# Kernel tuning notes

Hardware: AMD Instinct MI355X
Metric: run time of the kernel (lower is better)

Reference implementation:

```python
import jax, jax.numpy as jnp
import numpy as np

T = 16384
D_IN = 512
D_HID = 512
D_OUT = 512


def setup_inputs() -> dict:
    key = jax.random.key(0)
    ks = jax.random.split(key, 7)
    s_in = 1.0 / np.sqrt(D_IN)
    s_hid = 1.0 / np.sqrt(D_HID)
    xs = jax.random.normal(ks[0], (T, D_IN), dtype=jnp.float32)
    Wz = jax.random.uniform(ks[1], (D_HID, D_IN), jnp.float32, -s_in, s_in)
    bz = jax.random.uniform(ks[2], (D_HID,), jnp.float32, -s_in, s_in)
    Wh = jax.random.uniform(ks[3], (D_HID, D_IN), jnp.float32, -s_in, s_in)
    bh = jax.random.uniform(ks[4], (D_HID,), jnp.float32, -s_in, s_in)
    Wo = jax.random.uniform(ks[5], (D_OUT, D_HID), jnp.float32, -s_hid, s_hid)
    bo = jax.random.uniform(ks[6], (D_OUT,), jnp.float32, -s_hid, s_hid)
    return {"xs": xs, "Wz": Wz, "bz": bz, "Wh": Wh, "bh": bh, "Wo": Wo, "bo": bo}


def _combine(first, second):
    a0, b0 = first
    a1, b1 = second
    return (a0 * a1, a1 * b0 + b1)


def reference(xs, Wz, bz, Wh, bh, Wo, bo):
    # gates and candidate hidden states: [T, H]
    zs = jax.nn.sigmoid(xs @ Wz.T + bz)
    hs = xs @ Wh.T + bh
    # prepend identity element (a=1, b=0) for the h_0 = 0 initial state
    a = jnp.concatenate([jnp.ones((1, zs.shape[1]), zs.dtype), 1.0 - zs], axis=0)
    b = jnp.concatenate([jnp.zeros((1, zs.shape[1]), zs.dtype), zs * hs], axis=0)
    _, states = jax.lax.associative_scan(_combine, (a, b))  # [T+1, H]
    return states[1:] @ Wo.T + bo  # [T, D_OUT]
```

## Files before the change

### kernel.cpp

```cpp
#include <hip/hip_runtime.h>
#include <hip/hip_bf16.h>
#include <cstdint>
#include <cmath>

#define T_SEQ 16384
#define DMODEL 512
#define NCHUNK 512
#define LCHUNK 32
#define W_N    (DMODEL * DMODEL)
#define N4_W   (W_N / 4)
#define N4_W3  (3 * N4_W)

typedef __bf16 bf16x8 __attribute__((ext_vector_type(8)));
typedef float  f32x4  __attribute__((ext_vector_type(4)));

using bf16 = __hip_bfloat16;

__device__ __forceinline__ void load_lds16(const void* g, void* l) {
    __builtin_amdgcn_global_load_lds((const __attribute__((address_space(1))) void*)g,
                                     (__attribute__((address_space(3))) void*)l,
                                     16, 0, 0);
}

__device__ __forceinline__ unsigned short f2bf(float f) {
    union { float f; unsigned u; } v; v.f = f;
    const unsigned r = (v.u + 0x7FFFu + ((v.u >> 16) & 1u)) >> 16;
    return (unsigned short)r;
}
__device__ __forceinline__ float bf2f(unsigned short u) {
    union { unsigned u; float f; } v; v.u = ((unsigned)u) << 16;
    return v.f;
}

__device__ __forceinline__ void comb(float& A, float& B, float fA, float fB,
                                     float sA, float sB) {
    A = fA * sA;
    B = sA * fB + sB;
}

__global__ __launch_bounds__(256) void k_convert_w(
    const float* __restrict__ Wz, const float* __restrict__ Wh,
    const float* __restrict__ Wo,
    bf16* __restrict__ Wz_c, bf16* __restrict__ Wh_c, bf16* __restrict__ Wo_c)
{
    const int i = blockIdx.x * 256 + threadIdx.x;
    if (i >= N4_W3) return;
    const int w = i >> 16;
    const int o = i & 65535;
    const float* src = (w == 0) ? Wz : (w == 1) ? Wh : Wo;
    bf16* dst = (w == 0) ? Wz_c : (w == 1) ? Wh_c : Wo_c;
    const float4 v = ((const float4*)src)[o];
    ushort4 r;
    r.x = f2bf(v.x); r.y = f2bf(v.y); r.z = f2bf(v.z); r.w = f2bf(v.w);
    ((ushort4*)dst)[o] = r;
}

__global__ __launch_bounds__(256, 2) void gemm_zh(
    const float* __restrict__ xs, const bf16* __restrict__ Wz, const float* __restrict__ bz,
    const bf16* __restrict__ Wh, const float* __restrict__ bh,
    unsigned int* __restrict__ ab_ws,
    float* __restrict__ AaggT, float* __restrict__ BaggT)
{
    __shared__ __bf16 As[128 * 64];
    __shared__ __bf16 Zs[128 * 64];
    __shared__ __bf16 Hs[128 * 64];

    const int tid  = threadIdx.x;
    const int bm   = blockIdx.x;
    const int bn   = blockIdx.y;
    const int lane = tid & 63;
    const int wave = tid >> 6;
    const int wm   = wave >> 1;
    const int wn   = wave & 1;

    f32x4 accz[4][4], acch[4][4];
    #pragma unroll
    for (int i = 0; i < 4; ++i)
        #pragma unroll
        for (int j = 0; j < 4; ++j) {
            accz[i][j] = (f32x4){0.f, 0.f, 0.f, 0.f};
            acch[i][j] = (f32x4){0.f, 0.f, 0.f, 0.f};
        }

    const int row0 = tid >> 3;
    const int k8   = tid & 7;
    const bf16* zg = Wz + (size_t)(bn * 128) * DMODEL + k8 * 8;
    const bf16* hg = Wh + (size_t)(bn * 128) * DMODEL + k8 * 8;

    const int frow = tid >> 4;
    const int f4   = tid & 15;
    const float* xg = xs + ((size_t)(bm * 128) + frow) * DMODEL + f4 * 4;

    const int quad = lane >> 4;
    const int col  = lane & 15;

    for (int k0 = 0; k0 < DMODEL; k0 += 64) {
        #pragma unroll
        for (int it = 0; it < 4; ++it) {
            const int row   = row0 + it * 32;
            const int chunk = it * 256 + tid;
            load_lds16(zg + (size_t)row * DMODEL + k0, &Zs[chunk * 8]);
            load_lds16(hg + (size_t)row * DMODEL + k0, &Hs[chunk * 8]);
        }
        #pragma unroll
        for (int it2 = 0; it2 < 8; ++it2) {
            const int row = frow + it2 * 16;
            const float4 v = *(const float4*)(xg + (size_t)(it2 * 16) * DMODEL + k0);
            __hip_bfloat162 p0 = __float22bfloat162_rn(make_float2(v.x, v.y));
            __hip_bfloat162 p1 = __float22bfloat162_rn(make_float2(v.z, v.w));
            uint2 pk;
            pk.x = *(const unsigned*)&p0;
            pk.y = *(const unsigned*)&p1;
            *(uint2*)&As[row * 64 + f4 * 4] = pk;
        }
        __syncthreads();

        #pragma unroll
        for (int kk = 0; kk < 2; ++kk) {
            const int kb = kk * 32 + quad * 8;
            bf16x8 af[4], zf[4], hf[4];
            #pragma unroll
            for (int i = 0; i < 4; ++i) {
                const int am  = wm * 64 + i * 16 + col;
                const int bnr = wn * 64 + i * 16 + col;
                af[i] = *(const bf16x8*)&As[am * 64 + kb];
                zf[i] = *(const bf16x8*)&Zs[bnr * 64 + kb];
                hf[i] = *(const bf16x8*)&Hs[bnr * 64 + kb];
            }
            #pragma unroll
            for (int i = 0; i < 4; ++i)
                #pragma unroll
                for (int j = 0; j < 4; ++j) {
                    accz[i][j] = __builtin_amdgcn_mfma_f32_16x16x32_bf16(af[i], zf[j], accz[i][j], 0, 0, 0);
                    acch[i][j] = __builtin_amdgcn_mfma_f32_16x16x32_bf16(af[i], hf[j], acch[i][j], 0, 0, 0);
                }
        }
        __syncthreads();
    }

    const int c_lo = bm * 4 + wm * 2;
    #pragma unroll
    for (int j = 0; j < 4; ++j) {
        const int n = bn * 128 + wn * 64 + j * 16 + col;
        const float bzv = bz[n];
        const float bhv = bh[n];
        float cA[4], cB[4];
        #pragma unroll
        for (int i = 0; i < 4; ++i) {
            const int mbase = bm * 128 + wm * 64 + i * 16 + quad * 4;
            float A = 1.f, B = 0.f;
            #pragma unroll
            for (int r = 0; r < 4; ++r) {
                const float zpre = accz[i][j][r] + bzv;
                const float hpre = acch[i][j][r] + bhv;
                const float z = 1.f / (1.f + __expf(-zpre));
                const float a = 1.f - z;
                const float b = z * hpre;
                const size_t idx = (size_t)(mbase + r) * DMODEL + n;
                ab_ws[idx] = (unsigned)f2bf(a) | ((unsigned)f2bf(b) << 16);
                A = a * A;
                B = a * B + b;
            }
            cA[i] = A; cB[i] = B;
        }
        #pragma unroll
        for (int i = 0; i < 4; ++i) {
            float pA = __shfl_xor(cA[i], 16);
            float pB = __shfl_xor(cB[i], 16);
            const bool hi1 = quad & 1;
            comb(cA[i], cB[i], hi1 ? pA : cA[i], hi1 ? pB : cB[i],
                               hi1 ? cA[i] : pA, hi1 ? cB[i] : pB);
            pA = __shfl_xor(cA[i], 32);
            pB = __shfl_xor(cB[i], 32);
            const bool hi2 = quad >> 1;
            comb(cA[i], cB[i], hi2 ? pA : cA[i], hi2 ? pB : cB[i],
                               hi2 ? cA[i] : pA, hi2 ? cB[i] : pB);
        }
        float Alo, Blo, Ahi, Bhi;
        comb(Alo, Blo, cA[0], cB[0], cA[1], cB[1]);
        comb(Ahi, Bhi, cA[2], cB[2], cA[3], cB[3]);
        if (quad == 0) {
            AaggT[(size_t)n * NCHUNK + c_lo]     = Alo;
            BaggT[(size_t)n * NCHUNK + c_lo]     = Blo;
            AaggT[(size_t)n * NCHUNK + c_lo + 1] = Ahi;
            BaggT[(size_t)n * NCHUNK + c_lo + 1] = Bhi;
        }
    }
}

__global__ __launch_bounds__(512) void scan_p2(
    const float* __restrict__ AaggT, const float* __restrict__ BaggT,
    float* __restrict__ HpreT)
{
    const int h = blockIdx.x;
    const int c = threadIdx.x;
    __shared__ float sA[NCHUNK], sB[NCHUNK];

    float A = AaggT[(size_t)h * NCHUNK + c];
    float B = BaggT[(size_t)h * NCHUNK + c];
    sA[c] = A; sB[c] = B;
    __syncthreads();

    for (int off = 1; off < NCHUNK; off <<= 1) {
        float pA = 1.f, pB = 0.f;
        if (c >= off) { pA = sA[c - off]; pB = sB[c - off]; }
        __syncthreads();
        const float nB = A * pB + B;
        const float nA = A * pA;
        A = nA; B = nB;
        sA[c] = A; sB[c] = B;
        __syncthreads();
    }
    const float hp = (c == 0) ? 0.f : sB[c - 1];
    HpreT[(size_t)h * NCHUNK + c] = hp;
}

__global__ __launch_bounds__(256) void scan_p3(
    const unsigned int* __restrict__ ab_ws, const float* __restrict__ HpreT,
    unsigned short* __restrict__ states)
{
    const int tid = threadIdx.x;
    const int c   = blockIdx.x;
    float H0 = HpreT[(size_t)(2 * tid) * NCHUNK + c];
    float H1 = HpreT[(size_t)(2 * tid + 1) * NCHUNK + c];
    const size_t rowbase = (size_t)(c * LCHUNK) * DMODEL;
    #pragma unroll 8
    for (int i = 0; i < LCHUNK; ++i) {
        const size_t row = rowbase + (size_t)i * DMODEL;
        const uint2 u = ((const uint2*)(ab_ws + row))[tid];
        const float a0 = bf2f((unsigned short)(u.x & 0xFFFFu));
        const float b0 = bf2f((unsigned short)(u.x >> 16));
        const float a1 = bf2f((unsigned short)(u.y & 0xFFFFu));
        const float b1 = bf2f((unsigned short)(u.y >> 16));
        H0 = a0 * H0 + b0;
        H1 = a1 * H1 + b1;
        ushort2 s; s.x = f2bf(H0); s.y = f2bf(H1);
        ((ushort2*)(states + row))[tid] = s;
    }
}

__global__ __launch_bounds__(256, 2) void gemm_out(
    const bf16* __restrict__ states, const bf16* __restrict__ Wo, const float* __restrict__ bo,
    float* __restrict__ out)
{
    __shared__ __bf16 As[128 * 64];
    __shared__ __bf16 Bs[128 * 64];

    const int tid  = threadIdx.x;
    const int bm   = blockIdx.x;
    const int bn   = blockIdx.y;
    const int lane = tid & 63;
    const int wave = tid >> 6;
    const int wm   = wave >> 1;
    const int wn   = wave & 1;

    f32x4 acc[4][4];
    #pragma unroll
    for (int i = 0; i < 4; ++i)
        #pragma unroll
        for (int j = 0; j < 4; ++j)
            acc[i][j] = (f32x4){0.f, 0.f, 0.f, 0.f};

    const int row0 = tid >> 3;
    const int k8   = tid & 7;

    const bf16* ag = states + (size_t)(bm * 128) * DMODEL + k8 * 8;
    const bf16* bg = Wo     + (size_t)(bn * 128) * DMODEL + k8 * 8;

    const int quad = lane >> 4;
    const int col  = lane & 15;

    for (int k0 = 0; k0 < DMODEL; k0 += 64) {
        #pragma unroll
        for (int it = 0; it < 4; ++it) {
            const int row   = row0 + it * 32;
            const int chunk = it * 256 + tid;
            load_lds16(ag + (size_t)row * DMODEL + k0, &As[chunk * 8]);
            load_lds16(bg + (size_t)row * DMODEL + k0, &Bs[chunk * 8]);
        }
        __syncthreads();

        #pragma unroll
        for (int kk = 0; kk < 2; ++kk) {
            const int kb = kk * 32 + quad * 8;
            bf16x8 af[4], bf[4];
            #pragma unroll
            for (int i = 0; i < 4; ++i) {
                af[i] = *(const bf16x8*)&As[(wm * 64 + i * 16 + col) * 64 + kb];
                bf[i] = *(const bf16x8*)&Bs[(wn * 64 + i * 16 + col) * 64 + kb];
            }
            #pragma unroll
            for (int i = 0; i < 4; ++i)
                #pragma unroll
                for (int j = 0; j < 4; ++j)
                    acc[i][j] = __builtin_amdgcn_mfma_f32_16x16x32_bf16(af[i], bf[j], acc[i][j], 0, 0, 0);
        }
        __syncthreads();
    }

    #pragma unroll
    for (int j = 0; j < 4; ++j) {
        const int n = bn * 128 + wn * 64 + j * 16 + col;
        const float bov = bo[n];
        #pragma unroll
        for (int i = 0; i < 4; ++i) {
            const int mbase = bm * 128 + wm * 64 + i * 16 + quad * 4;
            #pragma unroll
            for (int r = 0; r < 4; ++r)
                out[(size_t)(mbase + r) * DMODEL + n] = acc[i][j][r] + bov;
        }
    }
}

extern "C" void kernel_launch(void* const* d_in, const int* in_sizes, int n_in,
                              void* d_out, int out_size, void* d_ws, size_t ws_size,
                              hipStream_t stream)
{
    const float* xs = (const float*)d_in[0];
    const float* Wz = (const float*)d_in[1];
    const float* bz = (const float*)d_in[2];
    const float* Wh = (const float*)d_in[3];
    const float* bh = (const float*)d_in[4];
    const float* Wo = (const float*)d_in[5];
    const float* bo = (const float*)d_in[6];
    float* out = (float*)d_out;

    char* w = (char*)d_ws;
    bf16*  Wz_c   = (bf16*) (w);
    bf16*  Wh_c   = (bf16*) (w + 524288ull);
    bf16*  Wo_c   = (bf16*) (w + 1048576ull);
    unsigned int*   ab_ws  = (unsigned int*)  (w + 1572864ull);
    unsigned short* states = (unsigned short*)(w + 35127296ull);
    float* AaggT  = (float*)(w + 51904512ull);
    float* BaggT  = (float*)(w + 52953088ull);
    float* HpreT  = (float*)(w + 54001664ull);

    k_convert_w<<<(N4_W3 + 255) / 256, 256, 0, stream>>>(Wz, Wh, Wo, Wz_c, Wh_c, Wo_c);
    gemm_zh<<<dim3(128, 4), 256, 0, stream>>>(xs, Wz_c, bz, Wh_c, bh, ab_ws, AaggT, BaggT);
    scan_p2<<<DMODEL, NCHUNK, 0, stream>>>(AaggT, BaggT, HpreT);
    scan_p3<<<NCHUNK, 256, 0, stream>>>(ab_ws, HpreT, states);
    gemm_out<<<dim3(128, 4), 256, 0, stream>>>((const bf16*)states, Wo_c, bo, out);
}
```

Measured before the change: 151.8 us.

## Fuse chunk-local scan and Wo bf16 conversion into the output GEMM

Removes the separate scan_p3 kernel. The output GEMM now rebuilds each 128x64 state tile in LDS by running the 32-step chunk recurrence from HpreT and the packed a/b workspace, so the bf16 states buffer is never written to or read back from global memory. Wo is also converted from fp32 to bf16 inside the GEMM load loop, which drops it from the conversion kernel. The cost is that each of the 4 column-blocks repeats the same scan, so the a/b workspace is read four times. The serial dependent loop and the synchronous Wo loads also replace the asynchronous global-to-LDS copies.

```diff
diff --git a/kernel.cpp b/kernel.cpp
--- a/kernel.cpp
+++ b/kernel.cpp
@@ -9,7 +9,7 @@
 #define LCHUNK 32
 #define W_N    (DMODEL * DMODEL)
 #define N4_W   (W_N / 4)
-#define N4_W3  (3 * N4_W)
+#define N4_W2  (2 * N4_W)
 
 typedef __bf16 bf16x8 __attribute__((ext_vector_type(8)));
 typedef float  f32x4  __attribute__((ext_vector_type(4)));
@@ -40,15 +40,14 @@
 
 __global__ __launch_bounds__(256) void k_convert_w(
     const float* __restrict__ Wz, const float* __restrict__ Wh,
-    const float* __restrict__ Wo,
-    bf16* __restrict__ Wz_c, bf16* __restrict__ Wh_c, bf16* __restrict__ Wo_c)
+    bf16* __restrict__ Wz_c, bf16* __restrict__ Wh_c)
 {
     const int i = blockIdx.x * 256 + threadIdx.x;
-    if (i >= N4_W3) return;
+    if (i >= N4_W2) return;
     const int w = i >> 16;
     const int o = i & 65535;
-    const float* src = (w == 0) ? Wz : (w == 1) ? Wh : Wo;
-    bf16* dst = (w == 0) ? Wz_c : (w == 1) ? Wh_c : Wo_c;
+    const float* src = (w == 0) ? Wz : Wh;
+    bf16* dst = (w == 0) ? Wz_c : Wh_c;
     const float4 v = ((const float4*)src)[o];
     ushort4 r;
     r.x = f2bf(v.x); r.y = f2bf(v.y); r.z = f2bf(v.z); r.w = f2bf(v.w);
@@ -215,32 +214,9 @@
     HpreT[(size_t)h * NCHUNK + c] = hp;
 }
 
-__global__ __launch_bounds__(256) void scan_p3(
+__global__ __launch_bounds__(256, 2) void gemm_out_fused(
     const unsigned int* __restrict__ ab_ws, const float* __restrict__ HpreT,
-    unsigned short* __restrict__ states)
-{
-    const int tid = threadIdx.x;
-    const int c   = blockIdx.x;
-    float H0 = HpreT[(size_t)(2 * tid) * NCHUNK + c];
-    float H1 = HpreT[(size_t)(2 * tid + 1) * NCHUNK + c];
-    const size_t rowbase = (size_t)(c * LCHUNK) * DMODEL;
-    #pragma unroll 8
-    for (int i = 0; i < LCHUNK; ++i) {
-        const size_t row = rowbase + (size_t)i * DMODEL;
-        const uint2 u = ((const uint2*)(ab_ws + row))[tid];
-        const float a0 = bf2f((unsigned short)(u.x & 0xFFFFu));
-        const float b0 = bf2f((unsigned short)(u.x >> 16));
-        const float a1 = bf2f((unsigned short)(u.y & 0xFFFFu));
-        const float b1 = bf2f((unsigned short)(u.y >> 16));
-        H0 = a0 * H0 + b0;
-        H1 = a1 * H1 + b1;
-        ushort2 s; s.x = f2bf(H0); s.y = f2bf(H1);
-        ((ushort2*)(states + row))[tid] = s;
-    }
-}
-
-__global__ __launch_bounds__(256, 2) void gemm_out(
-    const bf16* __restrict__ states, const bf16* __restrict__ Wo, const float* __restrict__ bo,
+    const float* __restrict__ Wo, const float* __restrict__ bo,
     float* __restrict__ out)
 {
     __shared__ __bf16 As[128 * 64];
@@ -261,22 +237,42 @@
         for (int j = 0; j < 4; ++j)
             acc[i][j] = (f32x4){0.f, 0.f, 0.f, 0.f};
 
-    const int row0 = tid >> 3;
-    const int k8   = tid & 7;
-
-    const bf16* ag = states + (size_t)(bm * 128) * DMODEL + k8 * 8;
-    const bf16* bg = Wo     + (size_t)(bn * 128) * DMODEL + k8 * 8;
+    const int frow = tid >> 4;
+    const int f4   = tid & 15;
+    const float* wg = Wo + ((size_t)(bn * 128) + frow) * DMODEL + f4 * 4;
+
+    const int cl = tid >> 6;
+    const int hl = tid & 63;
+    const int chunk = bm * 4 + cl;
+    const int tbase = chunk * LCHUNK;
 
     const int quad = lane >> 4;
     const int col  = lane & 15;
 
     for (int k0 = 0; k0 < DMODEL; k0 += 64) {
         #pragma unroll
-        for (int it = 0; it < 4; ++it) {
-            const int row   = row0 + it * 32;
-            const int chunk = it * 256 + tid;
-            load_lds16(ag + (size_t)row * DMODEL + k0, &As[chunk * 8]);
-            load_lds16(bg + (size_t)row * DMODEL + k0, &Bs[chunk * 8]);
+        for (int it2 = 0; it2 < 8; ++it2) {
+            const int row = frow + it2 * 16;
+            const float4 v = *(const float4*)(wg + (size_t)(it2 * 16) * DMODEL + k0);
+            __hip_bfloat162 p0 = __float22bfloat162_rn(make_float2(v.x, v.y));
+            __hip_bfloat162 p1 = __float22bfloat162_rn(make_float2(v.z, v.w));
+            uint2 pk;
+            pk.x = *(const unsigned*)&p0;
+            pk.y = *(const unsigned*)&p1;
+            *(uint2*)&Bs[row * 64 + f4 * 4] = pk;
+        }
+        {
+            const int h = k0 + hl;
+            float H = HpreT[(size_t)h * NCHUNK + chunk];
+            const unsigned int* ap = ab_ws + (size_t)tbase * DMODEL + h;
+            #pragma unroll 8
+            for (int i = 0; i < LCHUNK; ++i) {
+                const unsigned u = ap[(size_t)i * DMODEL];
+                const float a = bf2f((unsigned short)(u & 0xFFFFu));
+                const float b = bf2f((unsigned short)(u >> 16));
+                H = a * H + b;
+                *(unsigned short*)&As[(cl * LCHUNK + i) * 64 + hl] = f2bf(H);
+            }
         }
         __syncthreads();
 
@@ -328,16 +324,13 @@
     char* w = (char*)d_ws;
     bf16*  Wz_c   = (bf16*) (w);
     bf16*  Wh_c   = (bf16*) (w + 524288ull);
-    bf16*  Wo_c   = (bf16*) (w + 1048576ull);
-    unsigned int*   ab_ws  = (unsigned int*)  (w + 1572864ull);
-    unsigned short* states = (unsigned short*)(w + 35127296ull);
-    float* AaggT  = (float*)(w + 51904512ull);
-    float* BaggT  = (float*)(w + 52953088ull);
-    float* HpreT  = (float*)(w + 54001664ull);
-
-    k_convert_w<<<(N4_W3 + 255) / 256, 256, 0, stream>>>(Wz, Wh, Wo, Wz_c, Wh_c, Wo_c);
+    unsigned int* ab_ws = (unsigned int*)(w + 1048576ull);
+    float* AaggT  = (float*)(w + 34603008ull);
+    float* BaggT  = (float*)(w + 35651584ull);
+    float* HpreT  = (float*)(w + 36700160ull);
+
+    k_convert_w<<<(N4_W2 + 255) / 256, 256, 0, stream>>>(Wz, Wh, Wz_c, Wh_c);
     gemm_zh<<<dim3(128, 4), 256, 0, stream>>>(xs, Wz_c, bz, Wh_c, bh, ab_ws, AaggT, BaggT);
     scan_p2<<<DMODEL, NCHUNK, 0, stream>>>(AaggT, BaggT, HpreT);
-    scan_p3<<<NCHUNK, 256, 0, stream>>>(ab_ws, HpreT, states);
-    gemm_out<<<dim3(128, 4), 256, 0, stream>>>((const bf16*)states, Wo_c, bo, out);
-}
+    gemm_out_fused<<<dim3(128, 4), 256, 0, stream>>>(ab_ws, HpreT, Wo, bo, out);
+}
```

Measured after the change: 157.5 us. 1.04x slower.
